# Kernel optimization log

Hardware: AMD Instinct MI355X
Metric: run time of the kernel (lower is better)

## Reference

```python
import jax, jax.numpy as jnp
import numpy as np
import math

DK = 768  # latent_size used for the scale (not the per-head dim, matching the original)

def setup_inputs() -> dict:
    key = jax.random.key(0)
    k1, k2, k3 = jax.random.split(key, 3)
    B, H, S, D = 4, 12, 2048, 64
    queries = jax.random.normal(k1, (B, H, S, D), dtype=jnp.float32)
    keys = jax.random.normal(k2, (B, H, S, D), dtype=jnp.float32)
    values = jax.random.normal(k3, (B, S, H, D), dtype=jnp.float32)  # note [B,S,H,D] layout
    return {"queries": queries, "keys": keys, "values": values}

def reference(queries, keys, values):
    # scores: [B,H,S,S]
    scores = jnp.einsum('bhqd,bhkd->bhqk', queries, keys) / math.sqrt(DK)
    probs = jax.nn.softmax(scores, axis=3)
    v = jnp.transpose(values, (0, 2, 1, 3))  # [B,S,H,D] -> [B,H,S,D]
    return jnp.einsum('bhqk,bhkd->bhqd', probs, v)
```

## Files before the change

### kernel.cpp

```cpp
#include <hip/hip_runtime.h>

#define SQ 2048
#define DH 64
#define NH 12
#define NBH 48
#define QTILE 128
#define KTILE 64
#define NITER (SQ / KTILE)
#define NQT (SQ / QTILE)

typedef short short8 __attribute__((ext_vector_type(8)));
typedef float f32x4  __attribute__((ext_vector_type(4)));
typedef float f32x16 __attribute__((ext_vector_type(16)));
typedef int   i32x4 __attribute__((ext_vector_type(4)));

#define MFMA32(a, b, c) __builtin_amdgcn_mfma_f32_32x32x16_bf16(a, b, c, 0, 0, 0)

typedef __attribute__((address_space(1))) const void* gas_ptr;
typedef __attribute__((address_space(3))) void* las_ptr;

__device__ __forceinline__ void load_lds16(const void* g, void* l) {
    __builtin_amdgcn_global_load_lds((gas_ptr)g, (las_ptr)l, 16, 0, 0);
}

#if defined(__has_builtin) && __has_builtin(__builtin_amdgcn_cvt_pk_bf16_f32)
typedef __bf16 bf16x2_t __attribute__((ext_vector_type(2)));
__device__ __forceinline__ unsigned pk2bf(float a, float b) {
    bf16x2_t v = __builtin_amdgcn_cvt_pk_bf16_f32(a, b);
    union { bf16x2_t v; unsigned u; } c; c.v = v; return c.u;
}
#else
__device__ __forceinline__ unsigned pk2bf(float a, float b) {
    union { float f; unsigned u; } x, y; x.f = a; y.f = b;
    unsigned ra = x.u + 0x7FFFu + ((x.u >> 16) & 1u);
    unsigned rb = y.u + 0x7FFFu + ((y.u >> 16) & 1u);
    return (ra >> 16) | (rb & 0xFFFF0000u);
}
#endif

#define KCONV_BLOCKS (NBH * SQ * DH / 8 / 256)
__global__ __launch_bounds__(256)
void prepass(const float* __restrict__ K, short* __restrict__ Kb,
             const float* __restrict__ V, short* __restrict__ Vt) {
    __shared__ float Ls[64][68];
    if (blockIdx.x < KCONV_BLOCKS) {
        const size_t i = (size_t)(blockIdx.x * 256 + threadIdx.x) * 8;
        f32x4 a = *(const f32x4*)&K[i];
        f32x4 b = *(const f32x4*)&K[i + 4];
        unsigned o[4] = { pk2bf(a[0], a[1]), pk2bf(a[2], a[3]),
                          pk2bf(b[0], b[1]), pk2bf(b[2], b[3]) };
        *(i32x4*)&Kb[i] = *(i32x4*)o;
        return;
    }
    const int bx = blockIdx.x - KCONV_BLOCKS;
    const int st = bx & 31;
    const int bh = bx >> 5;
    const int b = bh / NH, h = bh % NH;
    const int s0 = st * 64;
    const float* src = V + ((size_t)b * SQ * NH + (size_t)h) * DH;
    const int dg = threadIdx.x & 15;
    const int sl = threadIdx.x >> 4;
    #pragma unroll
    for (int p = 0; p < 4; ++p) {
        const int row = p * 16 + sl;
        *(f32x4*)&Ls[row][dg * 4] =
            *(const f32x4*)&src[(size_t)(s0 + row) * (NH * DH) + dg * 4];
    }
    __syncthreads();
    const int dr = threadIdx.x >> 2;
    const int sc = (threadIdx.x & 3) * 16;
    unsigned out[8];
    #pragma unroll
    for (int jj = 0; jj < 8; ++jj)
        out[jj] = pk2bf(Ls[sc + 2 * jj][dr], Ls[sc + 2 * jj + 1][dr]);
    short* dst = Vt + (size_t)bh * DH * SQ + (size_t)dr * SQ + s0 + sc;
    *(i32x4*)(dst)     = *(i32x4*)&out[0];
    *(i32x4*)(dst + 8) = *(i32x4*)&out[4];
}

__global__ __launch_bounds__(256, 3)
void attn_fused_kernel(const float* __restrict__ Q,
                       const short* __restrict__ Kb,
                       const short* __restrict__ Vtg,
                       float* __restrict__ O) {
    __shared__ __align__(16) char L[32768];

    const int tid  = threadIdx.x;
    const int lane = tid & 63;
    const int w    = tid >> 6;
    const int m31  = lane & 31;
    const int hl   = lane >> 5;
    const int l7   = lane & 7;

    const int bx = blockIdx.x;
    const int qt = bx & (NQT - 1);
    const int bh = bx >> 4;
    const int q0 = qt * QTILE;

    const float* Qb  = Q   + (size_t)bh * SQ * DH;
    const short* Kbh = Kb  + (size_t)bh * SQ * DH;
    const short* Vbh = Vtg + (size_t)bh * DH * SQ;
    float*       Ob  = O   + (size_t)bh * SQ * DH;

    const float qscale = 0.03608439182435161f * 1.4426950408889634f;

    short8 qf[4];
    {
        const int qrow = q0 + 32 * w + m31;
        #pragma unroll
        for (int s = 0; s < 4; ++s) {
            const float* src = Qb + (size_t)qrow * DH + 16 * s + 8 * hl;
            f32x4 qa = *(const f32x4*)src;
            f32x4 qb = *(const f32x4*)(src + 4);
            union { unsigned u[4]; short8 v; } f;
            f.u[0] = pk2bf(qa[0] * qscale, qa[1] * qscale);
            f.u[1] = pk2bf(qa[2] * qscale, qa[3] * qscale);
            f.u[2] = pk2bf(qb[0] * qscale, qb[1] * qscale);
            f.u[3] = pk2bf(qb[2] * qscale, qb[3] * qscale);
            qf[s] = f.v;
        }
    }

    const int gk = (lane & 7) ^ (lane >> 3);
    const int rr = w * 8 + (lane >> 3);
    const short* kg0 = Kbh + (size_t)rr * DH + gk * 8;
    const short* kg1 = kg0 + 32 * DH;
    const short* vg0 = Vbh + (size_t)rr * SQ + gk * 8;
    const short* vg1 = vg0 + 32 * SQ;
    const int wslot = w * 1024;

    int aoff[4];
    #pragma unroll
    for (int s = 0; s < 4; ++s) aoff[s] = m31 * 128 + (((2 * s + hl) ^ l7) * 16);

    f32x16 o0 = {}, o1 = {};
    float lp = 0.f;

    auto issue = [&](int bb) {
        load_lds16(kg0, L + bb + wslot);
        load_lds16(kg1, L + bb + 4096 + wslot);
        load_lds16(vg0, L + bb + 8192 + wslot);
        load_lds16(vg1, L + bb + 12288 + wslot);
        kg0 += KTILE * DH; kg1 += KTILE * DH;
        vg0 += KTILE;      vg1 += KTILE;
    };

    auto softmax_pack = [&](const f32x16& sv, short8* dst) {
        #pragma unroll
        for (int wd = 0; wd < 2; ++wd) {
            float p[8];
            #pragma unroll
            for (int j = 0; j < 8; ++j)
                p[j] = __builtin_amdgcn_exp2f(sv[8 * wd + j]);
            lp += ((p[0] + p[1]) + (p[2] + p[3])) +
                  ((p[4] + p[5]) + (p[6] + p[7]));
            unsigned a0 = pk2bf(p[0], p[1]);
            unsigned a1 = pk2bf(p[2], p[3]);
            unsigned b0 = pk2bf(p[4], p[5]);
            unsigned b1 = pk2bf(p[6], p[7]);
            unsigned r0 = (unsigned)__shfl_xor((int)(hl ? a0 : b0), 32, 64);
            unsigned r1 = (unsigned)__shfl_xor((int)(hl ? a1 : b1), 32, 64);
            union { unsigned u[4]; short8 v; } fr;
            fr.u[0] = hl ? r0 : a0;
            fr.u[1] = hl ? r1 : a1;
            fr.u[2] = hl ? b0 : r0;
            fr.u[3] = hl ? b1 : r1;
            dst[wd] = fr.v;
        }
    };

    auto compute = [&](int bb) {
        f32x16 s0 = {}, s1 = {};
        #pragma unroll
        for (int s = 0; s < 4; ++s) {
            short8 ka0 = *(const short8*)(L + bb + aoff[s]);
            short8 ka1 = *(const short8*)(L + bb + 4096 + aoff[s]);
            s0 = MFMA32(ka0, qf[s], s0);
            s1 = MFMA32(ka1, qf[s], s1);
        }
        short8 pfrag[4];
        softmax_pack(s0, &pfrag[0]);
        softmax_pack(s1, &pfrag[2]);
        #pragma unroll
        for (int s = 0; s < 4; ++s) {
            short8 vb0 = *(const short8*)(L + bb + 8192 + aoff[s]);
            short8 vb1 = *(const short8*)(L + bb + 12288 + aoff[s]);
            o0 = MFMA32(pfrag[s], vb0, o0);
            o1 = MFMA32(pfrag[s], vb1, o1);
        }
    };

    issue(0);
    for (int it = 0; it < NITER; it += 2) {
        __syncthreads();
        issue(16384);
        compute(0);
        __syncthreads();
        if (it + 2 < NITER) issue(0);
        compute(16384);
    }

    float v = lp;
    v += __shfl_xor(v, 32, 64);
    const float linv = 1.0f / v;

    #pragma unroll
    for (int dt = 0; dt < 2; ++dt) {
        const f32x16& o = dt ? o1 : o0;
        #pragma unroll
        for (int reg = 0; reg < 16; ++reg) {
            const int qp = (reg & 3) + 8 * (reg >> 2) + 4 * hl;
            const float rl = __shfl(linv, qp, 64);
            const int q = q0 + 32 * w + qp;
            Ob[(size_t)q * DH + 32 * dt + m31] = o[reg] * rl;
        }
    }
}

extern "C" void kernel_launch(void* const* d_in, const int* in_sizes, int n_in,
                              void* d_out, int out_size, void* d_ws, size_t ws_size,
                              hipStream_t stream) {
    const float* Q = (const float*)d_in[0];
    const float* K = (const float*)d_in[1];
    const float* V = (const float*)d_in[2];
    float* O = (float*)d_out;

    short* Kb  = (short*)d_ws;
    short* Vtg = Kb + (size_t)NBH * SQ * DH;

    prepass<<<dim3(KCONV_BLOCKS + NBH * 32), dim3(256), 0, stream>>>(K, Kb, V, Vtg);
    attn_fused_kernel<<<dim3(NBH * NQT), dim3(256), 0, stream>>>(Q, Kb, Vtg, O);
}
```

Baseline: 177.2 us.

## Software-pipeline QK and PV across tiles with split K/V LDS buffers

Restructures the main loop so that each step computes QK^T for tile i while doing the PV MFMAs for tile i-1. K uses a double buffer and V a triple buffer in LDS (grown from 32 KB to 40 KB). The goal is to overlap the exp/softmax packing with MFMA work and keep only one barrier per tile. The larger LDS footprint may reduce how many blocks fit per CU, and the hand-unrolled buffer rotation must line up exactly with the tile count.

```diff
diff --git a/kernel.cpp b/kernel.cpp
--- a/kernel.cpp
+++ b/kernel.cpp
@@ -83,7 +83,7 @@
                        const short* __restrict__ Kb,
                        const short* __restrict__ Vtg,
                        float* __restrict__ O) {
-    __shared__ __align__(16) char L[32768];
+    __shared__ __align__(16) char L[40960];
 
     const int tid  = threadIdx.x;
     const int lane = tid & 63;
@@ -135,15 +135,7 @@
 
     f32x16 o0 = {}, o1 = {};
     float lp = 0.f;
-
-    auto issue = [&](int bb) {
-        load_lds16(kg0, L + bb + wslot);
-        load_lds16(kg1, L + bb + 4096 + wslot);
-        load_lds16(vg0, L + bb + 8192 + wslot);
-        load_lds16(vg1, L + bb + 12288 + wslot);
-        kg0 += KTILE * DH; kg1 += KTILE * DH;
-        vg0 += KTILE;      vg1 += KTILE;
-    };
+    short8 pfrag[4];
 
     auto softmax_pack = [&](const f32x16& sv, short8* dst) {
         #pragma unroll
@@ -169,36 +161,68 @@
         }
     };
 
-    auto compute = [&](int bb) {
+    #define ISSUE(KW, VW) do {                                   \
+        load_lds16(kg0, L + (KW) + wslot);                       \
+        load_lds16(kg1, L + (KW) + 4096 + wslot);                \
+        load_lds16(vg0, L + (VW) + wslot);                       \
+        load_lds16(vg1, L + (VW) + 4096 + wslot);                \
+        kg0 += KTILE * DH; kg1 += KTILE * DH;                    \
+        vg0 += KTILE;      vg1 += KTILE;                         \
+    } while (0)
+
+    #define STEP(KR, KW, VR, VW, DO_ISSUE) do {                                  \
+        __syncthreads();                                                         \
+        if (DO_ISSUE) ISSUE(KW, VW);                                             \
+        f32x16 s0 = {}, s1 = {};                                                 \
+        _Pragma("unroll")                                                        \
+        for (int s = 0; s < 4; ++s) {                                            \
+            short8 ka0 = *(const short8*)(L + (KR) + aoff[s]);                   \
+            short8 ka1 = *(const short8*)(L + (KR) + 4096 + aoff[s]);            \
+            short8 vb0 = *(const short8*)(L + (VR) + aoff[s]);                   \
+            short8 vb1 = *(const short8*)(L + (VR) + 4096 + aoff[s]);            \
+            s0 = MFMA32(ka0, qf[s], s0);                                         \
+            s1 = MFMA32(ka1, qf[s], s1);                                         \
+            o0 = MFMA32(pfrag[s], vb0, o0);                                      \
+            o1 = MFMA32(pfrag[s], vb1, o1);                                      \
+        }                                                                        \
+        softmax_pack(s0, &pfrag[0]);                                             \
+        softmax_pack(s1, &pfrag[2]);                                             \
+    } while (0)
+
+    ISSUE(0, 16384);
+    __syncthreads();
+    ISSUE(8192, 24576);
+    {
         f32x16 s0 = {}, s1 = {};
         #pragma unroll
         for (int s = 0; s < 4; ++s) {
-            short8 ka0 = *(const short8*)(L + bb + aoff[s]);
-            short8 ka1 = *(const short8*)(L + bb + 4096 + aoff[s]);
+            short8 ka0 = *(const short8*)(L + aoff[s]);
+            short8 ka1 = *(const short8*)(L + 4096 + aoff[s]);
             s0 = MFMA32(ka0, qf[s], s0);
             s1 = MFMA32(ka1, qf[s], s1);
         }
-        short8 pfrag[4];
         softmax_pack(s0, &pfrag[0]);
         softmax_pack(s1, &pfrag[2]);
-        #pragma unroll
-        for (int s = 0; s < 4; ++s) {
-            short8 vb0 = *(const short8*)(L + bb + 8192 + aoff[s]);
-            short8 vb1 = *(const short8*)(L + bb + 12288 + aoff[s]);
-            o0 = MFMA32(pfrag[s], vb0, o0);
-            o1 = MFMA32(pfrag[s], vb1, o1);
-        }
-    };
-
-    issue(0);
-    for (int it = 0; it < NITER; it += 2) {
-        __syncthreads();
-        issue(16384);
-        compute(0);
-        __syncthreads();
-        if (it + 2 < NITER) issue(0);
-        compute(16384);
-    }
+    }
+
+    for (int grp = 0; grp < 5; ++grp) {
+        STEP(8192, 0,    16384, 32768, 1);
+        STEP(0,    8192, 24576, 16384, 1);
+        STEP(8192, 0,    32768, 24576, 1);
+        STEP(0,    8192, 16384, 32768, 1);
+        STEP(8192, 0,    24576, 16384, 1);
+        STEP(0,    8192, 32768, 24576, 1);
+    }
+    STEP(8192, 0, 16384, 32768, 0);
+    #pragma unroll
+    for (int s = 0; s < 4; ++s) {
+        short8 vb0 = *(const short8*)(L + 24576 + aoff[s]);
+        short8 vb1 = *(const short8*)(L + 24576 + 4096 + aoff[s]);
+        o0 = MFMA32(pfrag[s], vb0, o0);
+        o1 = MFMA32(pfrag[s], vb1, o1);
+    }
+    #undef STEP
+    #undef ISSUE
 
     float v = lp;
     v += __shfl_xor(v, 32, 64);
```

After: 176.1 us. No clear change (-0.6%).

## Split key tiles across wave pairs with 64-row query tiles and LDS reduction

Applied to the files above, without the earlier changes.

Halves the query tile to 64 rows and has pairs of waves share a query block while each handles half of every 64-key tile. Partial outputs and row sums are combined through LDS at the end. This doubles the grid and halves LDS per block so more blocks fit per CU (launch bounds raised to 6). In exchange it drops the double-buffered K/V prefetch, adds two barriers per iteration, and makes each block reload K/V for fewer queries.

```diff
diff --git a/kernel.cpp b/kernel.cpp
--- a/kernel.cpp
+++ b/kernel.cpp
@@ -4,7 +4,7 @@
 #define DH 64
 #define NH 12
 #define NBH 48
-#define QTILE 128
+#define QTILE 64
 #define KTILE 64
 #define NITER (SQ / KTILE)
 #define NQT (SQ / QTILE)
@@ -78,24 +78,27 @@
     *(i32x4*)(dst + 8) = *(i32x4*)&out[4];
 }
 
-__global__ __launch_bounds__(256, 3)
+__global__ __launch_bounds__(256, 6)
 void attn_fused_kernel(const float* __restrict__ Q,
                        const short* __restrict__ Kb,
                        const short* __restrict__ Vtg,
                        float* __restrict__ O) {
-    __shared__ __align__(16) char L[32768];
+    __shared__ __align__(16) char L[16384];
+    __shared__ float lpb[2][64];
 
     const int tid  = threadIdx.x;
     const int lane = tid & 63;
     const int w    = tid >> 6;
     const int m31  = lane & 31;
     const int hl   = lane >> 5;
-    const int l7   = lane & 7;
+    const int l7   = m31 & 7;
+    const int h    = w & 1;
+    const int pr   = w >> 1;
 
     const int bx = blockIdx.x;
     const int qt = bx & (NQT - 1);
-    const int bh = bx >> 4;
-    const int q0 = qt * QTILE;
+    const int bh = bx >> 5;
+    const int q0 = qt * QTILE + 32 * pr;
 
     const float* Qb  = Q   + (size_t)bh * SQ * DH;
     const short* Kbh = Kb  + (size_t)bh * SQ * DH;
@@ -106,7 +109,7 @@
 
     short8 qf[4];
     {
-        const int qrow = q0 + 32 * w + m31;
+        const int qrow = q0 + m31;
         #pragma unroll
         for (int s = 0; s < 4; ++s) {
             const float* src = Qb + (size_t)qrow * DH + 16 * s + 8 * hl;
@@ -129,29 +132,42 @@
     const short* vg1 = vg0 + 32 * SQ;
     const int wslot = w * 1024;
 
-    int aoff[4];
-    #pragma unroll
-    for (int s = 0; s < 4; ++s) aoff[s] = m31 * 128 + (((2 * s + hl) ^ l7) * 16);
+    int kaoff[4];
+    #pragma unroll
+    for (int s = 0; s < 4; ++s)
+        kaoff[s] = (32 * h + m31) * 128 + (((2 * s + hl) ^ l7) * 16);
+    int voff[2];
+    #pragma unroll
+    for (int s = 0; s < 2; ++s)
+        voff[s] = m31 * 128 + (((2 * s + hl + 4 * h) ^ l7) * 16);
 
     f32x16 o0 = {}, o1 = {};
     float lp = 0.f;
 
-    auto issue = [&](int bb) {
-        load_lds16(kg0, L + bb + wslot);
-        load_lds16(kg1, L + bb + 4096 + wslot);
-        load_lds16(vg0, L + bb + 8192 + wslot);
-        load_lds16(vg1, L + bb + 12288 + wslot);
+    for (int it = 0; it < NITER; ++it) {
+        __syncthreads();
+        load_lds16(kg0, L + wslot);
+        load_lds16(kg1, L + 4096 + wslot);
+        load_lds16(vg0, L + 8192 + wslot);
+        load_lds16(vg1, L + 12288 + wslot);
         kg0 += KTILE * DH; kg1 += KTILE * DH;
         vg0 += KTILE;      vg1 += KTILE;
-    };
-
-    auto softmax_pack = [&](const f32x16& sv, short8* dst) {
+        __syncthreads();
+
+        f32x16 s0 = {};
+        #pragma unroll
+        for (int s = 0; s < 4; ++s) {
+            short8 ka = *(const short8*)(L + kaoff[s]);
+            s0 = MFMA32(ka, qf[s], s0);
+        }
+
+        short8 pfrag[2];
         #pragma unroll
         for (int wd = 0; wd < 2; ++wd) {
             float p[8];
             #pragma unroll
             for (int j = 0; j < 8; ++j)
-                p[j] = __builtin_amdgcn_exp2f(sv[8 * wd + j]);
+                p[j] = __builtin_amdgcn_exp2f(s0[8 * wd + j]);
             lp += ((p[0] + p[1]) + (p[2] + p[3])) +
                   ((p[4] + p[5]) + (p[6] + p[7]));
             unsigned a0 = pk2bf(p[0], p[1]);
@@ -165,54 +181,45 @@
             fr.u[1] = hl ? r1 : a1;
             fr.u[2] = hl ? b0 : r0;
             fr.u[3] = hl ? b1 : r1;
-            dst[wd] = fr.v;
-        }
-    };
-
-    auto compute = [&](int bb) {
-        f32x16 s0 = {}, s1 = {};
-        #pragma unroll
-        for (int s = 0; s < 4; ++s) {
-            short8 ka0 = *(const short8*)(L + bb + aoff[s]);
-            short8 ka1 = *(const short8*)(L + bb + 4096 + aoff[s]);
-            s0 = MFMA32(ka0, qf[s], s0);
-            s1 = MFMA32(ka1, qf[s], s1);
-        }
-        short8 pfrag[4];
-        softmax_pack(s0, &pfrag[0]);
-        softmax_pack(s1, &pfrag[2]);
-        #pragma unroll
-        for (int s = 0; s < 4; ++s) {
-            short8 vb0 = *(const short8*)(L + bb + 8192 + aoff[s]);
-            short8 vb1 = *(const short8*)(L + bb + 12288 + aoff[s]);
+            pfrag[wd] = fr.v;
+        }
+
+        #pragma unroll
+        for (int s = 0; s < 2; ++s) {
+            short8 vb0 = *(const short8*)(L + 8192 + voff[s]);
+            short8 vb1 = *(const short8*)(L + 12288 + voff[s]);
             o0 = MFMA32(pfrag[s], vb0, o0);
             o1 = MFMA32(pfrag[s], vb1, o1);
         }
-    };
-
-    issue(0);
-    for (int it = 0; it < NITER; it += 2) {
-        __syncthreads();
-        issue(16384);
-        compute(0);
-        __syncthreads();
-        if (it + 2 < NITER) issue(0);
-        compute(16384);
-    }
-
-    float v = lp;
-    v += __shfl_xor(v, 32, 64);
-    const float linv = 1.0f / v;
-
-    #pragma unroll
-    for (int dt = 0; dt < 2; ++dt) {
-        const f32x16& o = dt ? o1 : o0;
+    }
+
+    float vsum = lp + __shfl_xor(lp, 32, 64);
+    __syncthreads();
+    float* mb = (float*)L;
+    if (h) {
+        #pragma unroll
+        for (int i = 0; i < 16; ++i) {
+            mb[pr * 2048 + i * 64 + lane]        = o0[i];
+            mb[pr * 2048 + 1024 + i * 64 + lane] = o1[i];
+        }
+        lpb[pr][lane] = vsum;
+    }
+    __syncthreads();
+    if (!h) {
+        const float vtot = vsum + lpb[pr][lane];
+        const float linv = 1.0f / vtot;
+        #pragma unroll
+        for (int i = 0; i < 16; ++i) {
+            o0[i] += mb[pr * 2048 + i * 64 + lane];
+            o1[i] += mb[pr * 2048 + 1024 + i * 64 + lane];
+        }
         #pragma unroll
         for (int reg = 0; reg < 16; ++reg) {
             const int qp = (reg & 3) + 8 * (reg >> 2) + 4 * hl;
             const float rl = __shfl(linv, qp, 64);
-            const int q = q0 + 32 * w + qp;
-            Ob[(size_t)q * DH + 32 * dt + m31] = o[reg] * rl;
+            const int q = q0 + qp;
+            Ob[(size_t)q * DH + m31]      = o0[reg] * rl;
+            Ob[(size_t)q * DH + 32 + m31] = o1[reg] * rl;
         }
     }
 }
```

Measured after the change: 192.2 us. +8.5%, slower.
